# Performance work log

Hardware: AMD Instinct MI355X
Metric: run time of the kernel (lower is better)

The kernel has to match this reference:

```python
import jax, jax.numpy as jnp
import numpy as np

C = 256
CQK = C // 8  # 32


def setup_inputs() -> dict:
    key = jax.random.key(0)
    ks = jax.random.split(key, 7)
    x = jax.random.normal(ks[0], (4, C, 64, 64), dtype=jnp.float32)
    s = 1.0 / np.sqrt(C)
    Wq = jax.random.normal(ks[1], (CQK, C), dtype=jnp.float32) * s
    bq = jnp.zeros((CQK,), dtype=jnp.float32)
    Wk = jax.random.normal(ks[2], (CQK, C), dtype=jnp.float32) * s
    bk = jnp.zeros((CQK,), dtype=jnp.float32)
    Wv = jax.random.normal(ks[3], (C, C), dtype=jnp.float32) * s
    bv = jnp.zeros((C,), dtype=jnp.float32)
    return {"x": x, "Wq": Wq, "bq": bq, "Wk": Wk, "bk": bk, "Wv": Wv, "bv": bv}


def reference(x, Wq, bq, Wk, bk, Wv, bv):
    B, Cc, H, W = x.shape
    xf = x.reshape(B, Cc, H * W)  # [B, C, HW]
    # 1x1 convs == per-pixel linear projections over channels
    q = jnp.einsum('oc,bcn->bno', Wq, xf) + bq          # [B, HW, C//8]
    k = jnp.einsum('oc,bcn->bon', Wk, xf) + bk[:, None]  # [B, C//8, HW]
    v = jnp.einsum('oc,bcn->bno', Wv, xf) + bv          # [B, HW, C]
    attn = jax.nn.softmax(jnp.einsum('bnd,bdm->bnm', q, k), axis=-1)  # [B, HW, HW]
    out = jnp.einsum('bnm,bmc->bnc', attn, v)           # [B, HW, C]
    return out.transpose(0, 2, 1).reshape(B, Cc, H, W)
```

## Files before the change

kernel.cpp:

```cpp
#include <hip/hip_runtime.h>
#include <hip/hip_bf16.h>


#define N_PIX 4096
#define DQK   32
#define CCH   256
#define LOG2E 1.44269504088896f

typedef __attribute__((ext_vector_type(8))) _Float16 f16x8;
typedef __attribute__((ext_vector_type(4))) _Float16 f16x4;
typedef __attribute__((ext_vector_type(2))) _Float16 f16x2;
typedef __attribute__((ext_vector_type(8))) short    bf16x8;
typedef __attribute__((ext_vector_type(4))) short    bf16x4;
typedef __attribute__((ext_vector_type(4))) float    f32x4;

__device__ inline void barrier_lds() {
    asm volatile("" ::: "memory");
    __builtin_amdgcn_s_waitcnt(0xc07f);
    __builtin_amdgcn_s_barrier();
    asm volatile("" ::: "memory");
}

__device__ inline unsigned cvt_pk_bf16(float lo, float hi) {
    unsigned r;
    asm("v_cvt_pk_bf16_f32 %0, %1, %2" : "=v"(r) : "v"(lo), "v"(hi));
    return r;
}

__global__ __launch_bounds__(256) void wpack_kernel(
    const float* __restrict__ Wq, const float* __restrict__ Wk,
    const float* __restrict__ Wv, _Float16* __restrict__ Wp)
{
    const int tid   = threadIdx.x;
    const int wflat = blockIdx.x * 4 + (tid >> 6);
    const int lane  = tid & 63;
    const int L15   = lane & 15;
    const int quad  = lane >> 4;
    const int mt    = wflat >> 3;
    const int ks    = wflat & 7;
    const int m0    = mt * 16;

    const float* Wsrc; int row; float scale = 1.f;
    if (m0 < 32)      { Wsrc = Wq; row = m0 + L15;      scale = LOG2E; }
    else if (m0 < 64) { Wsrc = Wk; row = m0 - 32 + L15; }
    else              { Wsrc = Wv; row = m0 - 64 + L15; }

    const float* p = Wsrc + (size_t)row * 256 + ks * 32 + quad * 8;
    f16x8 h;
    #pragma unroll
    for (int j = 0; j < 8; ++j) h[j] = (_Float16)(p[j] * scale);
    *(f16x8*)(Wp + ((size_t)wflat * 64 + lane) * 8) = h;
}

__global__ __launch_bounds__(512, 4) void qkv_kernel(
    const float* __restrict__ x, const _Float16* __restrict__ Wp,
    const float* __restrict__ bq, const float* __restrict__ bk,
    const float* __restrict__ bv,
    _Float16* __restrict__ qo, _Float16* __restrict__ ko,
    __hip_bfloat16* __restrict__ vp)
{
    __shared__ alignas(16) unsigned char shraw[256 * 40 * 2];
    _Float16       (*xT)[264] = (_Float16 (*)[264])shraw;
    __hip_bfloat16 (*vst)[40] = (__hip_bfloat16 (*)[40])shraw;

    const int idx = blockIdx.x;
    const int b   = (idx & 7) >> 1;
    const int n0  = (((idx >> 3) << 1) | (idx & 1)) * 32;
    const int tid = threadIdx.x;

    {
        const float* xb = x + (size_t)b * CCH * N_PIX;
        float4 ld[2][2];
        int c2s[2], n4s[2];
        #pragma unroll
        for (int pass = 0; pass < 2; ++pass) {
            const int flat = pass * 512 + tid;
            c2s[pass] = (flat >> 3) * 2;
            n4s[pass] = (flat & 7) * 4;
            ld[pass][0] = *(const float4*)(xb + (size_t)c2s[pass]       * N_PIX + n0 + n4s[pass]);
            ld[pass][1] = *(const float4*)(xb + (size_t)(c2s[pass] + 1) * N_PIX + n0 + n4s[pass]);
        }
        #pragma unroll
        for (int pass = 0; pass < 2; ++pass) {
            const float a[4] = {ld[pass][0].x, ld[pass][0].y, ld[pass][0].z, ld[pass][0].w};
            const float c[4] = {ld[pass][1].x, ld[pass][1].y, ld[pass][1].z, ld[pass][1].w};
            #pragma unroll
            for (int i = 0; i < 4; ++i)
                *(f16x2*)(&xT[n4s[pass] + i][c2s[pass]]) =
                    (f16x2){(_Float16)a[i], (_Float16)c[i]};
        }
    }
    __syncthreads();

    const int lane = tid & 63;
    const int wid  = tid >> 6;
    const int L15  = lane & 15;
    const int quad = lane >> 4;
    const int nf   = wid & 1;
    const int mtg  = wid >> 1;

    const f32x4 fz = {0.f, 0.f, 0.f, 0.f};
    f32x4 acc[5];
    #pragma unroll
    for (int mt = 0; mt < 5; ++mt) acc[mt] = fz;

    const _Float16* wpw = Wp + ((size_t)(mtg * 5) * 8 * 64 + lane) * 8;

    #pragma unroll
    for (int ks = 0; ks < 8; ++ks) {
        const f16x8 bfr = *(const f16x8*)(&xT[nf * 16 + L15][ks * 32 + quad * 8]);
        #pragma unroll
        for (int mt = 0; mt < 5; ++mt) {
            const f16x8 afr = *(const f16x8*)(wpw + (size_t)(mt * 8 + ks) * 512);
            acc[mt] = __builtin_amdgcn_mfma_f32_16x16x32_f16(afr, bfr, acc[mt], 0, 0, 0);
        }
    }

    const int np = nf * 16 + L15;
    const int n  = n0 + np;
    #pragma unroll
    for (int mt = 0; mt < 5; ++mt) {
        const int m0 = (mtg * 5 + mt) * 16;
        const f32x4 a = acc[mt];
        if (m0 < 32) {
            const int mr = m0 + quad * 4;
            f16x4 h;
            #pragma unroll
            for (int r = 0; r < 4; ++r) h[r] = (_Float16)(a[r] + bq[mr + r] * LOG2E);
            *(f16x4*)(qo + ((size_t)b * N_PIX + n) * DQK + mr) = h;
        } else if (m0 < 64) {
            const int mr = m0 - 32 + quad * 4;
            f16x4 h;
            #pragma unroll
            for (int r = 0; r < 4; ++r) h[r] = (_Float16)(a[r] + bk[mr + r]);
            *(f16x4*)(ko + ((size_t)b * N_PIX + n) * DQK + mr) = h;
        }
    }

    __syncthreads();

    #pragma unroll
    for (int mt = 0; mt < 5; ++mt) {
        const int m0 = (mtg * 5 + mt) * 16;
        if (m0 >= 64) {
            const int c = m0 - 64 + quad * 4;
            #pragma unroll
            for (int r = 0; r < 4; ++r)
                vst[c + r][np] = __float2bfloat16(acc[mt][r] + bv[c + r]);
        }
    }
    __syncthreads();

    {
        __hip_bfloat16* vpb = vp + (size_t)b * 2048 * 512 + (size_t)((n0 >> 5) * 16) * 512;
        #pragma unroll
        for (int s = 0; s < 2; ++s) {
            const int slot = s * 512 + tid;
            const int cg16 = slot >> 6;
            const int ln   = slot & 63;
            const int qd   = ln >> 4;
            const int l15  = ln & 15;
            const bf16x8 val = *(const bf16x8*)(&vst[cg16 * 16 + l15][qd * 8]);
            *(bf16x8*)(vpb + ((size_t)cg16 * 64 + ln) * 8) = val;
        }
    }
}


#define PV_BODY(J, VR)                                                            \
  {                                                                               \
    const int buf_ = (J) & 1;                                                     \
    _Pragma("unroll")                                                             \
    for (int qq_ = 0; qq_ < 4; ++qq_) {                                           \
      _Pragma("unroll")                                                           \
      for (int kk_ = 0; kk_ < 2; ++kk_) {                                         \
        const bf16x8 ap_ = *(const bf16x8*)(&Ps[buf_][qq_ * 2 + kk_][quad][L15][0]); \
        oacc[qq_][0] = __builtin_amdgcn_mfma_f32_16x16x32_bf16(                   \
            ap_, VR[kk_][0], oacc[qq_][0], 0, 0, 0);                              \
        oacc[qq_][1] = __builtin_amdgcn_mfma_f32_16x16x32_bf16(                   \
            ap_, VR[kk_][1], oacc[qq_][1], 0, 0, 0);                              \
      }                                                                           \
    }                                                                             \
    const __hip_bfloat16* vt_ = vb + (size_t)(((J) + 2) & 63) * 16384;            \
    _Pragma("unroll")                                                             \
    for (int kk_ = 0; kk_ < 2; ++kk_)                                             \
      _Pragma("unroll")                                                           \
      for (int cf_ = 0; cf_ < 2; ++cf_)                                           \
        VR[kk_][cf_] = *(const bf16x8*)(vt_ + voff0 + kk_ * 8192 + cf_ * 512);    \
  }

#define S_BODY(J, KR0, KR1, DO_S)                                                 \
  {                                                                               \
    if (DO_S) {                                                                   \
      const int bufw_ = ((J) & 1) ^ 1;                                            \
      const f32x4 s0_ = __builtin_amdgcn_mfma_f32_16x16x32_f16(KR0, aq, fz, 0, 0, 0); \
      const f32x4 s1_ = __builtin_amdgcn_mfma_f32_16x16x32_f16(KR1, aq, fz, 0, 0, 0); \
      const _Float16* kp_ = kbp + (size_t)(((J) + 3) & 63) * (64 * DQK);          \
      KR0 = *(const f16x8*)(kp_ + koff0);                                         \
      KR1 = *(const f16x8*)(kp_ + koff1);                                         \
      const float a0_ = exp2f(s0_[0]), a1_ = exp2f(s0_[1]);                       \
      const float a2_ = exp2f(s0_[2]), a3_ = exp2f(s0_[3]);                       \
      psum0 += (a0_ + a1_) + (a2_ + a3_);                                         \
      uint2 w0_; w0_.x = cvt_pk_bf16(a0_, a1_); w0_.y = cvt_pk_bf16(a2_, a3_);    \
      *(uint2*)(&Ps[bufw_][grp][quad >> 1][L15][(quad & 1) * 4]) = w0_;           \
      const float b0_ = exp2f(s1_[0]), b1_ = exp2f(s1_[1]);                       \
      const float b2_ = exp2f(s1_[2]), b3_ = exp2f(s1_[3]);                       \
      psum1 += (b0_ + b1_) + (b2_ + b3_);                                         \
      uint2 w1_; w1_.x = cvt_pk_bf16(b0_, b1_); w1_.y = cvt_pk_bf16(b2_, b3_);    \
      *(uint2*)(&Ps[bufw_][grp][2 + (quad >> 1)][L15][(quad & 1) * 4]) = w1_;     \
    }                                                                             \
  }

__global__ __launch_bounds__(1024, 4) void attn_kernel(
    const _Float16* __restrict__ qg,
    const _Float16* __restrict__ kg,
    const __hip_bfloat16* __restrict__ vp,
    float* __restrict__ out)
{
    __shared__ __hip_bfloat16 Ps[2][8][4][16][8];
    __shared__ float lsum[4][4][16];

    const int idx  = blockIdx.x;
    const int b    = (idx & 7) >> 1;
    const int n0   = (((idx >> 3) << 1) | (idx & 1)) * 64;
    const int tid  = threadIdx.x;
    const int wid  = tid >> 6;
    const int lane = tid & 63;
    const int L15  = lane & 15;
    const int quad = lane >> 4;
    const bool is_pv = (wid < 8);

    const f32x4 fz = {0.f, 0.f, 0.f, 0.f};

    const int cg = wid & 7;
    const __hip_bfloat16* vb = vp + (size_t)b * 2048 * 512;
    const int voff0 = lane * 8 + cg * 2 * 512;
    f32x4 oacc[4][2];
    #pragma unroll
    for (int qq = 0; qq < 4; ++qq) { oacc[qq][0] = fz; oacc[qq][1] = fz; }
    bf16x8 vA[2][2], vB[2][2];

    const int sqt  = (wid & 7) >> 1;
    const int kt0  = (wid & 1) * 2;
    const int grp  = wid & 7;
    const _Float16* kbp = kg + (size_t)b * N_PIX * DQK;
    const int koff0 = ((kt0 + 0) * 16 + L15) * DQK + quad * 8;
    const int koff1 = ((kt0 + 1) * 16 + L15) * DQK + quad * 8;
    f16x8 aq{}, kA0{}, kA1{}, kB0{}, kB1{};
    float psum0 = 0.f, psum1 = 0.f;

    if (is_pv) {
        #pragma unroll
        for (int kk = 0; kk < 2; ++kk)
            #pragma unroll
            for (int cf = 0; cf < 2; ++cf) {
                vA[kk][cf] = *(const bf16x8*)(vb +         voff0 + kk * 8192 + cf * 512);
                vB[kk][cf] = *(const bf16x8*)(vb + 16384 + voff0 + kk * 8192 + cf * 512);
            }
    } else {
        aq = *(const f16x8*)(qg + ((size_t)b * N_PIX + n0 + sqt * 16 + L15) * DQK + quad * 8);
        const f16x8 k00 = *(const f16x8*)(kbp + koff0);
        const f16x8 k01 = *(const f16x8*)(kbp + koff1);
        kA0 = *(const f16x8*)(kbp + (size_t)1 * 64 * DQK + koff0);
        kA1 = *(const f16x8*)(kbp + (size_t)1 * 64 * DQK + koff1);
        kB0 = *(const f16x8*)(kbp + (size_t)2 * 64 * DQK + koff0);
        kB1 = *(const f16x8*)(kbp + (size_t)2 * 64 * DQK + koff1);
        const f32x4 s0 = __builtin_amdgcn_mfma_f32_16x16x32_f16(k00, aq, fz, 0, 0, 0);
        const f32x4 s1 = __builtin_amdgcn_mfma_f32_16x16x32_f16(k01, aq, fz, 0, 0, 0);
        const float a0 = exp2f(s0[0]), a1 = exp2f(s0[1]);
        const float a2 = exp2f(s0[2]), a3 = exp2f(s0[3]);
        psum0 += (a0 + a1) + (a2 + a3);
        uint2 w0; w0.x = cvt_pk_bf16(a0, a1); w0.y = cvt_pk_bf16(a2, a3);
        *(uint2*)(&Ps[0][grp][quad >> 1][L15][(quad & 1) * 4]) = w0;
        const float b0 = exp2f(s1[0]), b1 = exp2f(s1[1]);
        const float b2 = exp2f(s1[2]), b3 = exp2f(s1[3]);
        psum1 += (b0 + b1) + (b2 + b3);
        uint2 w1; w1.x = cvt_pk_bf16(b0, b1); w1.y = cvt_pk_bf16(b2, b3);
        *(uint2*)(&Ps[0][grp][2 + (quad >> 1)][L15][(quad & 1) * 4]) = w1;
    }
    barrier_lds();

    for (int it = 0; it < 64; it += 2) {
        if (is_pv) { PV_BODY(it, vA) } else { S_BODY(it, kA0, kA1, true) }
        barrier_lds();
        if (is_pv) { PV_BODY(it + 1, vB) } else { S_BODY(it + 1, kB0, kB1, it < 62) }
        barrier_lds();
    }

    if (!is_pv) {
        psum0 += __shfl_xor(psum0, 16, 64);
        psum0 += __shfl_xor(psum0, 32, 64);
        psum1 += __shfl_xor(psum1, 16, 64);
        psum1 += __shfl_xor(psum1, 32, 64);
        if (quad == 0) {
            lsum[sqt][kt0 + 0][L15] = psum0;
            lsum[sqt][kt0 + 1][L15] = psum1;
        }
    }
    __syncthreads();

    if (is_pv) {
        float* ob = out + (size_t)b * CCH * N_PIX;
        #pragma unroll
        for (int qq = 0; qq < 4; ++qq) {
            float inv_l[4];
            #pragma unroll
            for (int r = 0; r < 4; ++r) {
                const int q = quad * 4 + r;
                inv_l[r] = 1.f / (lsum[qq][0][q] + lsum[qq][1][q] +
                                  lsum[qq][2][q] + lsum[qq][3][q]);
            }
            #pragma unroll
            for (int cf = 0; cf < 2; ++cf) {
                const int c = cg * 32 + cf * 16 + L15;
                f32x4 o;
                #pragma unroll
                for (int r = 0; r < 4; ++r) o[r] = oacc[qq][cf][r] * inv_l[r];
                *(f32x4*)(ob + (size_t)c * N_PIX + n0 + qq * 16 + quad * 4) = o;
            }
        }
    }
}

extern "C" void kernel_launch(void* const* d_in, const int* in_sizes, int n_in,
                              void* d_out, int out_size, void* d_ws, size_t ws_size,
                              hipStream_t stream) {
    (void)in_sizes; (void)n_in; (void)out_size; (void)ws_size;
    const float* x  = (const float*)d_in[0];
    const float* Wq = (const float*)d_in[1];
    const float* bq = (const float*)d_in[2];
    const float* Wk = (const float*)d_in[3];
    const float* bk = (const float*)d_in[4];
    const float* Wv = (const float*)d_in[5];
    const float* bv = (const float*)d_in[6];

    _Float16* qb = (_Float16*)d_ws;
    _Float16* kb = qb + (size_t)4 * N_PIX * DQK;
    __hip_bfloat16* vpk = (__hip_bfloat16*)(kb + (size_t)4 * N_PIX * DQK);
    _Float16* wp = (_Float16*)(vpk + (size_t)4 * 2048 * 512);
    float* outp = (float*)d_out;

    wpack_kernel<<<40, 256, 0, stream>>>(Wq, Wk, Wv, wp);
    qkv_kernel<<<512, 512, 0, stream>>>(x, wp, bq, bk, bv, qb, kb, vpk);
    attn_kernel<<<256, 1024, 0, stream>>>(qb, kb, vpk, outp);
}
```

Before: 140.3 us.

## Process two key tiles per barrier and retile PV warps over query halves

The P-tile LDS buffer grows from two slots to four, so the score warps can produce two key tiles per step and the PV warps can consume two tiles per step. This halves the number of workgroup barriers in the main loop. The PV warps are also remapped: each one now covers half of the queries and 64 channels, instead of all queries and 32 channels. That halves the LDS reads of P per warp but doubles its V register footprint (more VGPRs held in vA/vB), which could pressure occupancy under the 1024-thread launch bound.

Result: slower. 246.2 us (+75.5%).

```diff
diff --git a/kernel.cpp b/kernel.cpp
--- a/kernel.cpp
+++ b/kernel.cpp
@@ -169,46 +169,41 @@
 
 #define PV_BODY(J, VR)                                                            \
   {                                                                               \
-    const int buf_ = (J) & 1;                                                     \
+    const int buf_ = (J) & 3;                                                     \
     _Pragma("unroll")                                                             \
-    for (int qq_ = 0; qq_ < 4; ++qq_) {                                           \
+    for (int q2_ = 0; q2_ < 2; ++q2_) {                                           \
       _Pragma("unroll")                                                           \
       for (int kk_ = 0; kk_ < 2; ++kk_) {                                         \
-        const bf16x8 ap_ = *(const bf16x8*)(&Ps[buf_][qq_ * 2 + kk_][quad][L15][0]); \
-        oacc[qq_][0] = __builtin_amdgcn_mfma_f32_16x16x32_bf16(                   \
-            ap_, VR[kk_][0], oacc[qq_][0], 0, 0, 0);                              \
-        oacc[qq_][1] = __builtin_amdgcn_mfma_f32_16x16x32_bf16(                   \
-            ap_, VR[kk_][1], oacc[qq_][1], 0, 0, 0);                              \
+        const bf16x8 ap_ = *(const bf16x8*)(                                      \
+            &Ps[buf_][(qh * 2 + q2_) * 2 + kk_][quad][L15][0]);                   \
+        _Pragma("unroll")                                                         \
+        for (int cf_ = 0; cf_ < 4; ++cf_)                                         \
+          oacc[q2_][cf_] = __builtin_amdgcn_mfma_f32_16x16x32_bf16(               \
+              ap_, VR[kk_][cf_], oacc[q2_][cf_], 0, 0, 0);                        \
       }                                                                           \
     }                                                                             \
     const __hip_bfloat16* vt_ = vb + (size_t)(((J) + 2) & 63) * 16384;            \
     _Pragma("unroll")                                                             \
     for (int kk_ = 0; kk_ < 2; ++kk_)                                             \
       _Pragma("unroll")                                                           \
-      for (int cf_ = 0; cf_ < 2; ++cf_)                                           \
-        VR[kk_][cf_] = *(const bf16x8*)(vt_ + voff0 + kk_ * 8192 + cf_ * 512);    \
+      for (int cf_ = 0; cf_ < 4; ++cf_)                                           \
+        VR[kk_][cf_] = *(const bf16x8*)(vt_ + voffW + kk_ * 8192 + cf_ * 512);    \
   }
 
-#define S_BODY(J, KR0, KR1, DO_S)                                                 \
+#define S_TILE(KR0, KR1, BUF)                                                     \
   {                                                                               \
-    if (DO_S) {                                                                   \
-      const int bufw_ = ((J) & 1) ^ 1;                                            \
-      const f32x4 s0_ = __builtin_amdgcn_mfma_f32_16x16x32_f16(KR0, aq, fz, 0, 0, 0); \
-      const f32x4 s1_ = __builtin_amdgcn_mfma_f32_16x16x32_f16(KR1, aq, fz, 0, 0, 0); \
-      const _Float16* kp_ = kbp + (size_t)(((J) + 3) & 63) * (64 * DQK);          \
-      KR0 = *(const f16x8*)(kp_ + koff0);                                         \
-      KR1 = *(const f16x8*)(kp_ + koff1);                                         \
-      const float a0_ = exp2f(s0_[0]), a1_ = exp2f(s0_[1]);                       \
-      const float a2_ = exp2f(s0_[2]), a3_ = exp2f(s0_[3]);                       \
-      psum0 += (a0_ + a1_) + (a2_ + a3_);                                         \
-      uint2 w0_; w0_.x = cvt_pk_bf16(a0_, a1_); w0_.y = cvt_pk_bf16(a2_, a3_);    \
-      *(uint2*)(&Ps[bufw_][grp][quad >> 1][L15][(quad & 1) * 4]) = w0_;           \
-      const float b0_ = exp2f(s1_[0]), b1_ = exp2f(s1_[1]);                       \
-      const float b2_ = exp2f(s1_[2]), b3_ = exp2f(s1_[3]);                       \
-      psum1 += (b0_ + b1_) + (b2_ + b3_);                                         \
-      uint2 w1_; w1_.x = cvt_pk_bf16(b0_, b1_); w1_.y = cvt_pk_bf16(b2_, b3_);    \
-      *(uint2*)(&Ps[bufw_][grp][2 + (quad >> 1)][L15][(quad & 1) * 4]) = w1_;     \
-    }                                                                             \
+    const f32x4 s0_ = __builtin_amdgcn_mfma_f32_16x16x32_f16(KR0, aq, fz, 0, 0, 0); \
+    const f32x4 s1_ = __builtin_amdgcn_mfma_f32_16x16x32_f16(KR1, aq, fz, 0, 0, 0); \
+    const float a0_ = exp2f(s0_[0]), a1_ = exp2f(s0_[1]);                         \
+    const float a2_ = exp2f(s0_[2]), a3_ = exp2f(s0_[3]);                         \
+    psum0 += (a0_ + a1_) + (a2_ + a3_);                                           \
+    uint2 w0_; w0_.x = cvt_pk_bf16(a0_, a1_); w0_.y = cvt_pk_bf16(a2_, a3_);      \
+    *(uint2*)(&Ps[BUF][grp][quad >> 1][L15][(quad & 1) * 4]) = w0_;               \
+    const float b0_ = exp2f(s1_[0]), b1_ = exp2f(s1_[1]);                         \
+    const float b2_ = exp2f(s1_[2]), b3_ = exp2f(s1_[3]);                         \
+    psum1 += (b0_ + b1_) + (b2_ + b3_);                                           \
+    uint2 w1_; w1_.x = cvt_pk_bf16(b0_, b1_); w1_.y = cvt_pk_bf16(b2_, b3_);      \
+    *(uint2*)(&Ps[BUF][grp][2 + (quad >> 1)][L15][(quad & 1) * 4]) = w1_;         \
   }
 
 __global__ __launch_bounds__(1024, 4) void attn_kernel(
@@ -217,7 +212,7 @@
     const __hip_bfloat16* __restrict__ vp,
     float* __restrict__ out)
 {
-    __shared__ __hip_bfloat16 Ps[2][8][4][16][8];
+    __shared__ __hip_bfloat16 Ps[4][8][4][16][8];
     __shared__ float lsum[4][4][16];
 
     const int idx  = blockIdx.x;
@@ -232,13 +227,16 @@
 
     const f32x4 fz = {0.f, 0.f, 0.f, 0.f};
 
-    const int cg = wid & 7;
+    const int qh   = wid & 1;
+    const int cgrp = wid >> 1;
     const __hip_bfloat16* vb = vp + (size_t)b * 2048 * 512;
-    const int voff0 = lane * 8 + cg * 2 * 512;
-    f32x4 oacc[4][2];
-    #pragma unroll
-    for (int qq = 0; qq < 4; ++qq) { oacc[qq][0] = fz; oacc[qq][1] = fz; }
-    bf16x8 vA[2][2], vB[2][2];
+    const int voffW = lane * 8 + (cgrp * 4) * 512;
+    f32x4 oacc[2][4];
+    #pragma unroll
+    for (int q2 = 0; q2 < 2; ++q2)
+        #pragma unroll
+        for (int cf = 0; cf < 4; ++cf) oacc[q2][cf] = fz;
+    bf16x8 vA[2][4], vB[2][4];
 
     const int sqt  = (wid & 7) >> 1;
     const int kt0  = (wid & 1) * 2;
@@ -253,37 +251,47 @@
         #pragma unroll
         for (int kk = 0; kk < 2; ++kk)
             #pragma unroll
-            for (int cf = 0; cf < 2; ++cf) {
-                vA[kk][cf] = *(const bf16x8*)(vb +         voff0 + kk * 8192 + cf * 512);
-                vB[kk][cf] = *(const bf16x8*)(vb + 16384 + voff0 + kk * 8192 + cf * 512);
+            for (int cf = 0; cf < 4; ++cf) {
+                vA[kk][cf] = *(const bf16x8*)(vb +         voffW + kk * 8192 + cf * 512);
+                vB[kk][cf] = *(const bf16x8*)(vb + 16384 + voffW + kk * 8192 + cf * 512);
             }
     } else {
         aq = *(const f16x8*)(qg + ((size_t)b * N_PIX + n0 + sqt * 16 + L15) * DQK + quad * 8);
-        const f16x8 k00 = *(const f16x8*)(kbp + koff0);
-        const f16x8 k01 = *(const f16x8*)(kbp + koff1);
-        kA0 = *(const f16x8*)(kbp + (size_t)1 * 64 * DQK + koff0);
-        kA1 = *(const f16x8*)(kbp + (size_t)1 * 64 * DQK + koff1);
-        kB0 = *(const f16x8*)(kbp + (size_t)2 * 64 * DQK + koff0);
-        kB1 = *(const f16x8*)(kbp + (size_t)2 * 64 * DQK + koff1);
-        const f32x4 s0 = __builtin_amdgcn_mfma_f32_16x16x32_f16(k00, aq, fz, 0, 0, 0);
-        const f32x4 s1 = __builtin_amdgcn_mfma_f32_16x16x32_f16(k01, aq, fz, 0, 0, 0);
-        const float a0 = exp2f(s0[0]), a1 = exp2f(s0[1]);
-        const float a2 = exp2f(s0[2]), a3 = exp2f(s0[3]);
-        psum0 += (a0 + a1) + (a2 + a3);
-        uint2 w0; w0.x = cvt_pk_bf16(a0, a1); w0.y = cvt_pk_bf16(a2, a3);
-        *(uint2*)(&Ps[0][grp][quad >> 1][L15][(quad & 1) * 4]) = w0;
-        const float b0 = exp2f(s1[0]), b1 = exp2f(s1[1]);
-        const float b2 = exp2f(s1[2]), b3 = exp2f(s1[3]);
-        psum1 += (b0 + b1) + (b2 + b3);
-        uint2 w1; w1.x = cvt_pk_bf16(b0, b1); w1.y = cvt_pk_bf16(b2, b3);
-        *(uint2*)(&Ps[0][grp][2 + (quad >> 1)][L15][(quad & 1) * 4]) = w1;
+        {
+            const f16x8 k00 = *(const f16x8*)(kbp + koff0);
+            const f16x8 k01 = *(const f16x8*)(kbp + koff1);
+            S_TILE(k00, k01, 0)
+        }
+        {
+            const f16x8 k10 = *(const f16x8*)(kbp + (size_t)64 * DQK + koff0);
+            const f16x8 k11 = *(const f16x8*)(kbp + (size_t)64 * DQK + koff1);
+            S_TILE(k10, k11, 1)
+        }
+        kA0 = *(const f16x8*)(kbp + (size_t)2 * 64 * DQK + koff0);
+        kA1 = *(const f16x8*)(kbp + (size_t)2 * 64 * DQK + koff1);
+        kB0 = *(const f16x8*)(kbp + (size_t)3 * 64 * DQK + koff0);
+        kB1 = *(const f16x8*)(kbp + (size_t)3 * 64 * DQK + koff1);
     }
     barrier_lds();
 
     for (int it = 0; it < 64; it += 2) {
-        if (is_pv) { PV_BODY(it, vA) } else { S_BODY(it, kA0, kA1, true) }
-        barrier_lds();
-        if (is_pv) { PV_BODY(it + 1, vB) } else { S_BODY(it + 1, kB0, kB1, it < 62) }
+        if (is_pv) {
+            PV_BODY(it,     vA)
+            PV_BODY(it + 1, vB)
+        } else if (it < 62) {
+            S_TILE(kA0, kA1, (it + 2) & 3)
+            {
+                const _Float16* kp = kbp + (size_t)((it + 4) & 63) * (64 * DQK);
+                kA0 = *(const f16x8*)(kp + koff0);
+                kA1 = *(const f16x8*)(kp + koff1);
+            }
+            S_TILE(kB0, kB1, (it + 3) & 3)
+            {
+                const _Float16* kp = kbp + (size_t)((it + 5) & 63) * (64 * DQK);
+                kB0 = *(const f16x8*)(kp + koff0);
+                kB1 = *(const f16x8*)(kp + koff1);
+            }
+        }
         barrier_lds();
     }
 
@@ -302,21 +310,22 @@
     if (is_pv) {
         float* ob = out + (size_t)b * CCH * N_PIX;
         #pragma unroll
-        for (int qq = 0; qq < 4; ++qq) {
+        for (int q2 = 0; q2 < 2; ++q2) {
+            const int qtile = qh * 2 + q2;
             float inv_l[4];
             #pragma unroll
             for (int r = 0; r < 4; ++r) {
                 const int q = quad * 4 + r;
-                inv_l[r] = 1.f / (lsum[qq][0][q] + lsum[qq][1][q] +
-                                  lsum[qq][2][q] + lsum[qq][3][q]);
-            }
-            #pragma unroll
-            for (int cf = 0; cf < 2; ++cf) {
-                const int c = cg * 32 + cf * 16 + L15;
+                inv_l[r] = 1.f / (lsum[qtile][0][q] + lsum[qtile][1][q] +
+                                  lsum[qtile][2][q] + lsum[qtile][3][q]);
+            }
+            #pragma unroll
+            for (int cf = 0; cf < 4; ++cf) {
+                const int c = cgrp * 64 + cf * 16 + L15;
                 f32x4 o;
                 #pragma unroll
-                for (int r = 0; r < 4; ++r) o[r] = oacc[qq][cf][r] * inv_l[r];
-                *(f32x4*)(ob + (size_t)c * N_PIX + n0 + qq * 16 + quad * 4) = o;
+                for (int r = 0; r < 4; ++r) o[r] = oacc[q2][cf][r] * inv_l[r];
+                *(f32x4*)(ob + (size_t)c * N_PIX + n0 + qtile * 16 + quad * 4) = o;
             }
         }
     }
```
